# Optimization experiments

Measured on AMD Instinct MI355X. Metric: run time of the kernel, lower is better.

## Reference

```python
import jax, jax.numpy as jnp
import numpy as np

ALPHA = 0.2          # LeakyReLU negative slope
NEG_INF = -9e15      # mask value used by the torch module


def setup_inputs() -> dict:
    key = jax.random.key(0)
    k1, k2, k3, k4 = jax.random.split(key, 4)
    N, F_IN, F_OUT = 8192, 128, 128
    h = jax.random.normal(k1, (N, F_IN), dtype=jnp.float32)
    adj = jax.random.randint(k2, (N, N), 0, 2, dtype=jnp.int32)
    # xavier_uniform(gain=1.414) approximated with scaled normal init
    W = jax.random.normal(k3, (F_IN, F_OUT), dtype=jnp.float32) * (1.414 / np.sqrt(F_IN))
    a = jax.random.normal(k4, (2 * F_OUT, 1), dtype=jnp.float32) * (1.414 / np.sqrt(2 * F_OUT))
    return {"h": h, "adj": adj, "W": W, "a": a}


def reference(h, adj, W, a):
    # Wh: [N, F]
    Wh = h @ W
    F_out = W.shape[1]
    # e[i,j] = LeakyReLU( [Wh_i || Wh_j] . a ) = LeakyReLU( Wh_i.a1 + Wh_j.a2 )
    e_src = Wh @ a[:F_out, 0]   # [N]
    e_dst = Wh @ a[F_out:, 0]   # [N]
    e = jax.nn.leaky_relu(e_src[:, None] + e_dst[None, :], negative_slope=ALPHA)  # [N, N]
    attention = jax.nn.softmax(jnp.where(adj > 0, e, NEG_INF), axis=1)
    # dropout is identity in eval mode
    h_prime = attention @ Wh    # [N, F]
    return h_prime
```

## Files before the change

### kernel.cpp

```cpp
#include <hip/hip_runtime.h>
#include <hip/hip_bf16.h>


#define NN 8192
#define FF 128
#define SEG 4
#define JSEG (NN / SEG)
#define ITERS (JSEG / 64)

typedef __bf16 bf16x8 __attribute__((ext_vector_type(8)));
typedef float floatx4 __attribute__((ext_vector_type(4)));

__device__ __forceinline__ unsigned short f2b(float f) {
    unsigned int u = __float_as_uint(f);
    return (unsigned short)((u + 0x7FFFu + ((u >> 16) & 1u)) >> 16);
}

__global__ __launch_bounds__(128) void k0_uv(const float* __restrict__ W,
                                             const float* __restrict__ a,
                                             float* __restrict__ u,
                                             float* __restrict__ v) {
    int k = blockIdx.x, t = threadIdx.x;
    float wv = W[k * FF + t];
    float p1 = wv * a[t];
    float p2 = wv * a[FF + t];
    for (int off = 32; off; off >>= 1) {
        p1 += __shfl_down(p1, off);
        p2 += __shfl_down(p2, off);
    }
    __shared__ float r[4];
    if ((t & 63) == 0) { r[(t >> 6) * 2] = p1; r[(t >> 6) * 2 + 1] = p2; }
    __syncthreads();
    if (t == 0) { u[k] = r[0] + r[2]; v[k] = r[1] + r[3]; }
}

__global__ __launch_bounds__(256) void k1_wh(const float* __restrict__ h,
                                             const float* __restrict__ W,
                                             const float* __restrict__ u,
                                             const float* __restrict__ v,
                                             unsigned short* __restrict__ WhT,
                                             float* __restrict__ e_src,
                                             float* __restrict__ e_dst) {
    __shared__ float hL[32 * 132];
    __shared__ float wL[128 * 132];
    __shared__ float uL[128], vL[128];
    __shared__ unsigned short tL[128 * 40];

    int t = threadIdx.x;
    int i0 = blockIdx.x * 32;

    {
        int row = t >> 3, c = (t & 7) * 16;
        const float4* s = (const float4*)&h[(i0 + row) * FF + c];
        float4* d = (float4*)&hL[row * 132 + c];
        #pragma unroll
        for (int j = 0; j < 4; j++) d[j] = s[j];
    }
    {
        int row = t >> 1, c = (t & 1) * 64;
        const float4* s = (const float4*)&W[row * FF + c];
        float4* d = (float4*)&wL[row * 132 + c];
        #pragma unroll
        for (int j = 0; j < 16; j++) d[j] = s[j];
    }
    if (t < 128) { uL[t] = u[t]; vL[t] = v[t]; }
    __syncthreads();

    int r0 = (t & 7) * 4;
    int c0 = (t >> 3) * 4;
    float acc[4][4] = {};
    for (int k0 = 0; k0 < 128; k0 += 4) {
        float4 hr[4], wr[4];
        #pragma unroll
        for (int i = 0; i < 4; i++) hr[i] = *(const float4*)&hL[(r0 + i) * 132 + k0];
        #pragma unroll
        for (int i = 0; i < 4; i++) wr[i] = *(const float4*)&wL[(k0 + i) * 132 + c0];
        #pragma unroll
        for (int kj = 0; kj < 4; kj++) {
            #pragma unroll
            for (int ri = 0; ri < 4; ri++) {
                float hvv = ((const float*)&hr[ri])[kj];
                const float* wvv = (const float*)&wr[kj];
                #pragma unroll
                for (int cj = 0; cj < 4; cj++) acc[ri][cj] = fmaf(hvv, wvv[cj], acc[ri][cj]);
            }
        }
    }
    #pragma unroll
    for (int ri = 0; ri < 4; ri++)
        #pragma unroll
        for (int cj = 0; cj < 4; cj++)
            tL[(c0 + cj) * 40 + r0 + ri] = f2b(acc[ri][cj]);
    __syncthreads();

    if (t < 64) {
        int row = t & 31;
        const float* sv = (t < 32) ? uL : vL;
        float s = 0.f;
        for (int k = 0; k < 128; k += 4) {
            float4 h4 = *(const float4*)&hL[row * 132 + k];
            float4 s4 = *(const float4*)&sv[k];
            s = fmaf(h4.x, s4.x, s); s = fmaf(h4.y, s4.y, s);
            s = fmaf(h4.z, s4.z, s); s = fmaf(h4.w, s4.w, s);
        }
        (t < 32 ? e_src : e_dst)[i0 + row] = s;
    }
    {
        int f = t & 127, half = t >> 7;
        const uint4* s = (const uint4*)&tL[f * 40 + half * 16];
        uint4* d = (uint4*)&WhT[f * NN + i0 + half * 16];
        d[0] = s[0]; d[1] = s[1];
    }
}

__device__ __forceinline__ float mask_w(int a, float x) {
    float l = fmaxf(x, 0.2f * x);
    return a > 0 ? __expf(l) : 0.f;
}

__global__ __launch_bounds__(512, 4) void k2_gat(const int* __restrict__ adj,
                                                 const unsigned short* __restrict__ WhT,
                                                 const float* __restrict__ e_src,
                                                 const float* __restrict__ e_dst,
                                                 float* __restrict__ numpart,
                                                 float* __restrict__ denpart) {
    __shared__ unsigned short wt[2][32 * 64];
    __shared__ float esL[32];
    __shared__ float dpart[32 * 17];

    int t = threadIdx.x;
    int bx = blockIdx.x;
    int g = bx >> 2, seg = bx & 3;
    int i0 = g * 32;
    int jbase = seg * JSEG;

    if (t < 32) esL[t] = e_src[i0 + t];

    int q  = t & 15;
    int ii = t >> 4;
    int lane = t & 63, wave = t >> 6;
    int mrow = lane & 15, quad = lane >> 4;
    int n0 = wave * 16;

    const unsigned short* Bb = WhT + (size_t)(n0 + mrow) * NN + jbase + quad * 8;
    const int*   Ab = adj + (size_t)(i0 + ii) * NN + jbase + q * 4;
    const float* Eb = e_dst + jbase + q * 4;

    int waddr = ii * 64 + (((q >> 1) ^ (ii & 7)) << 3) + ((q & 1) << 2);
    int ra00 = mrow * 64 + ((quad ^ (mrow & 7)) << 3);
    int ra01 = mrow * 64 + (((4 + quad) ^ (mrow & 7)) << 3);
    int ra10 = (16 + mrow) * 64 + ((quad ^ (mrow & 7)) << 3);
    int ra11 = (16 + mrow) * 64 + (((4 + quad) ^ (mrow & 7)) << 3);

    floatx4 acc0 = {0.f, 0.f, 0.f, 0.f};
    floatx4 acc1 = {0.f, 0.f, 0.f, 0.f};
    float dsum = 0.f;

    int4   av0 = *(const int4*)Ab;
    float4 ed0 = *(const float4*)Eb;
    int4   avB = *(const int4*)(Ab + 64);
    float4 edB = *(const float4*)(Eb + 64);
    bf16x8 b0 = *(const bf16x8*)Bb;
    bf16x8 b1 = *(const bf16x8*)(Bb + 32);

    __syncthreads();
    float es_i = esL[ii];

    {
        float w0 = mask_w(av0.x, es_i + ed0.x);
        float w1 = mask_w(av0.y, es_i + ed0.y);
        float w2 = mask_w(av0.z, es_i + ed0.z);
        float w3 = mask_w(av0.w, es_i + ed0.w);
        dsum += (w0 + w1) + (w2 + w3);
        *(ushort4*)&wt[0][waddr] = make_ushort4(f2b(w0), f2b(w1), f2b(w2), f2b(w3));
    }
    __syncthreads();

    for (int k = 0; k < ITERS - 1; k++) {
        int jp = ((k + 2 < ITERS) ? (k + 2) : (ITERS - 1)) * 64;
        int4   avN = *(const int4*)(Ab + jp);
        float4 edN = *(const float4*)(Eb + jp);
        int jn = (k + 1) * 64;
        bf16x8 nb0 = *(const bf16x8*)(Bb + jn);
        bf16x8 nb1 = *(const bf16x8*)(Bb + jn + 32);

        const unsigned short* buf = wt[k & 1];
        bf16x8 a00 = *(const bf16x8*)&buf[ra00];
        bf16x8 a10 = *(const bf16x8*)&buf[ra10];
        bf16x8 a01 = *(const bf16x8*)&buf[ra01];
        bf16x8 a11 = *(const bf16x8*)&buf[ra11];
        acc0 = __builtin_amdgcn_mfma_f32_16x16x32_bf16(a00, b0, acc0, 0, 0, 0);
        acc1 = __builtin_amdgcn_mfma_f32_16x16x32_bf16(a10, b0, acc1, 0, 0, 0);
        acc0 = __builtin_amdgcn_mfma_f32_16x16x32_bf16(a01, b1, acc0, 0, 0, 0);
        acc1 = __builtin_amdgcn_mfma_f32_16x16x32_bf16(a11, b1, acc1, 0, 0, 0);

        float w0 = mask_w(avB.x, es_i + edB.x);
        float w1 = mask_w(avB.y, es_i + edB.y);
        float w2 = mask_w(avB.z, es_i + edB.z);
        float w3 = mask_w(avB.w, es_i + edB.w);
        dsum += (w0 + w1) + (w2 + w3);
        *(ushort4*)&wt[(k + 1) & 1][waddr] = make_ushort4(f2b(w0), f2b(w1), f2b(w2), f2b(w3));
        avB = avN; edB = edN;
        b0 = nb0; b1 = nb1;
        __syncthreads();
    }
    {
        const unsigned short* buf = wt[(ITERS - 1) & 1];
        bf16x8 a00 = *(const bf16x8*)&buf[ra00];
        bf16x8 a10 = *(const bf16x8*)&buf[ra10];
        bf16x8 a01 = *(const bf16x8*)&buf[ra01];
        bf16x8 a11 = *(const bf16x8*)&buf[ra11];
        acc0 = __builtin_amdgcn_mfma_f32_16x16x32_bf16(a00, b0, acc0, 0, 0, 0);
        acc1 = __builtin_amdgcn_mfma_f32_16x16x32_bf16(a10, b0, acc1, 0, 0, 0);
        acc0 = __builtin_amdgcn_mfma_f32_16x16x32_bf16(a01, b1, acc0, 0, 0, 0);
        acc1 = __builtin_amdgcn_mfma_f32_16x16x32_bf16(a11, b1, acc1, 0, 0, 0);
    }

    dpart[ii * 17 + q] = dsum;
    __syncthreads();
    if (t < 32) {
        float s = 0.f;
        #pragma unroll
        for (int k = 0; k < 16; k++) s += dpart[t * 17 + k];
        __builtin_nontemporal_store(s, &denpart[seg * NN + i0 + t]);
    }

    float* np = numpart + (size_t)seg * NN * FF;
    #pragma unroll
    for (int r = 0; r < 4; r++) {
        int row0 = quad * 4 + r;
        __builtin_nontemporal_store(acc0[r], &np[(size_t)(i0 + row0) * FF + n0 + mrow]);
        __builtin_nontemporal_store(acc1[r], &np[(size_t)(i0 + 16 + row0) * FF + n0 + mrow]);
    }
}

__global__ __launch_bounds__(256) void k3_merge(const float* __restrict__ np,
                                               const float* __restrict__ dp,
                                               float* __restrict__ out) {
    int idx = blockIdx.x * 256 + threadIdx.x;
    int i = idx >> 5;
    int c = (idx & 31) << 2;
    float d = dp[i] + dp[NN + i] + dp[2 * NN + i] + dp[3 * NN + i];
    float r = 1.0f / d;
    size_t o = (size_t)i * FF + c;
    const size_t S = (size_t)NN * FF;
    float4 a0 = *(const float4*)&np[o];
    float4 a1 = *(const float4*)&np[o + S];
    float4 a2 = *(const float4*)&np[o + 2 * S];
    float4 a3 = *(const float4*)&np[o + 3 * S];
    float4 v;
    v.x = ((a0.x + a1.x) + (a2.x + a3.x)) * r;
    v.y = ((a0.y + a1.y) + (a2.y + a3.y)) * r;
    v.z = ((a0.z + a1.z) + (a2.z + a3.z)) * r;
    v.w = ((a0.w + a1.w) + (a2.w + a3.w)) * r;
    *(float4*)&out[o] = v;
}

extern "C" void kernel_launch(void* const* d_in, const int* in_sizes, int n_in,
                              void* d_out, int out_size, void* d_ws, size_t ws_size,
                              hipStream_t stream) {
    const float* h   = (const float*)d_in[0];
    const int*   adj = (const int*)d_in[1];
    const float* W   = (const float*)d_in[2];
    const float* a   = (const float*)d_in[3];
    float* out = (float*)d_out;

    char* ws = (char*)d_ws;
    unsigned short* WhT = (unsigned short*)ws;
    float* u     = (float*)(ws + 2097152);
    float* v     = u + 128;
    float* e_src = v + 128;
    float* e_dst = e_src + NN;
    float* denpart = e_dst + NN;
    float* numpart = (float*)(ws + (4u << 20));

    k0_uv<<<dim3(128), dim3(128), 0, stream>>>(W, a, u, v);
    k1_wh<<<dim3(256), dim3(256), 0, stream>>>(h, W, u, v, WhT, e_src, e_dst);
    k2_gat<<<dim3(256 * SEG), dim3(512), 0, stream>>>(adj, WhT, e_src, e_dst, numpart, denpart);
    k3_merge<<<dim3(NN * FF / 4 / 256), dim3(256), 0, stream>>>(numpart, denpart, out);
}
```

Baseline: 404.3 us.

## Fuse uv projection into Wh kernel, use exp2, hardware bf16 cvt, nontemporal adj loads

```diff
diff --git a/kernel.cpp b/kernel.cpp
--- a/kernel.cpp
+++ b/kernel.cpp
@@ -10,34 +10,15 @@
 
 typedef __bf16 bf16x8 __attribute__((ext_vector_type(8)));
 typedef float floatx4 __attribute__((ext_vector_type(4)));
-
-__device__ __forceinline__ unsigned short f2b(float f) {
-    unsigned int u = __float_as_uint(f);
-    return (unsigned short)((u + 0x7FFFu + ((u >> 16) & 1u)) >> 16);
-}
-
-__global__ __launch_bounds__(128) void k0_uv(const float* __restrict__ W,
+typedef int   intx4  __attribute__((ext_vector_type(4)));
+
+__device__ __forceinline__ unsigned short b2u(__bf16 x) {
+    return __builtin_bit_cast(unsigned short, x);
+}
+
+__global__ __launch_bounds__(512) void k1_wh(const float* __restrict__ h,
+                                             const float* __restrict__ W,
                                              const float* __restrict__ a,
-                                             float* __restrict__ u,
-                                             float* __restrict__ v) {
-    int k = blockIdx.x, t = threadIdx.x;
-    float wv = W[k * FF + t];
-    float p1 = wv * a[t];
-    float p2 = wv * a[FF + t];
-    for (int off = 32; off; off >>= 1) {
-        p1 += __shfl_down(p1, off);
-        p2 += __shfl_down(p2, off);
-    }
-    __shared__ float r[4];
-    if ((t & 63) == 0) { r[(t >> 6) * 2] = p1; r[(t >> 6) * 2 + 1] = p2; }
-    __syncthreads();
-    if (t == 0) { u[k] = r[0] + r[2]; v[k] = r[1] + r[3]; }
-}
-
-__global__ __launch_bounds__(256) void k1_wh(const float* __restrict__ h,
-                                             const float* __restrict__ W,
-                                             const float* __restrict__ u,
-                                             const float* __restrict__ v,
                                              unsigned short* __restrict__ WhT,
                                              float* __restrict__ e_src,
                                              float* __restrict__ e_dst) {
@@ -50,47 +31,56 @@
     int i0 = blockIdx.x * 32;
 
     {
-        int row = t >> 3, c = (t & 7) * 16;
+        int row = t >> 4, c = (t & 15) * 8;
         const float4* s = (const float4*)&h[(i0 + row) * FF + c];
         float4* d = (float4*)&hL[row * 132 + c];
-        #pragma unroll
-        for (int j = 0; j < 4; j++) d[j] = s[j];
-    }
-    {
-        int row = t >> 1, c = (t & 1) * 64;
+        d[0] = s[0]; d[1] = s[1];
+    }
+    {
+        int row = t >> 2, c = (t & 3) * 32;
         const float4* s = (const float4*)&W[row * FF + c];
         float4* d = (float4*)&wL[row * 132 + c];
         #pragma unroll
-        for (int j = 0; j < 16; j++) d[j] = s[j];
-    }
-    if (t < 128) { uL[t] = u[t]; vL[t] = v[t]; }
-    __syncthreads();
+        for (int j = 0; j < 8; j++) d[j] = s[j];
+    }
+    __syncthreads();
+
+    if (t < 256) {
+        int k = t & 127;
+        const float* ap = a + (t >> 7) * FF;
+        float s = 0.f;
+        for (int c = 0; c < 128; c += 4) {
+            float4 w4 = *(const float4*)&wL[k * 132 + c];
+            s = fmaf(w4.x, ap[c], s);     s = fmaf(w4.y, ap[c + 1], s);
+            s = fmaf(w4.z, ap[c + 2], s); s = fmaf(w4.w, ap[c + 3], s);
+        }
+        (t < 128 ? uL : vL)[k] = s * 1.44269504f;
+    }
 
     int r0 = (t & 7) * 4;
-    int c0 = (t >> 3) * 4;
-    float acc[4][4] = {};
+    int c0 = (t >> 3) * 2;
+    float acc[4][2] = {};
     for (int k0 = 0; k0 < 128; k0 += 4) {
-        float4 hr[4], wr[4];
+        float4 hr[4]; float2 wr[4];
         #pragma unroll
         for (int i = 0; i < 4; i++) hr[i] = *(const float4*)&hL[(r0 + i) * 132 + k0];
         #pragma unroll
-        for (int i = 0; i < 4; i++) wr[i] = *(const float4*)&wL[(k0 + i) * 132 + c0];
+        for (int i = 0; i < 4; i++) wr[i] = *(const float2*)&wL[(k0 + i) * 132 + c0];
         #pragma unroll
         for (int kj = 0; kj < 4; kj++) {
             #pragma unroll
             for (int ri = 0; ri < 4; ri++) {
                 float hvv = ((const float*)&hr[ri])[kj];
-                const float* wvv = (const float*)&wr[kj];
-                #pragma unroll
-                for (int cj = 0; cj < 4; cj++) acc[ri][cj] = fmaf(hvv, wvv[cj], acc[ri][cj]);
+                acc[ri][0] = fmaf(hvv, wr[kj].x, acc[ri][0]);
+                acc[ri][1] = fmaf(hvv, wr[kj].y, acc[ri][1]);
             }
         }
     }
     #pragma unroll
     for (int ri = 0; ri < 4; ri++)
         #pragma unroll
-        for (int cj = 0; cj < 4; cj++)
-            tL[(c0 + cj) * 40 + r0 + ri] = f2b(acc[ri][cj]);
+        for (int cj = 0; cj < 2; cj++)
+            tL[(c0 + cj) * 40 + r0 + ri] = b2u((__bf16)acc[ri][cj]);
     __syncthreads();
 
     if (t < 64) {
@@ -106,16 +96,24 @@
         (t < 32 ? e_src : e_dst)[i0 + row] = s;
     }
     {
-        int f = t & 127, half = t >> 7;
-        const uint4* s = (const uint4*)&tL[f * 40 + half * 16];
-        uint4* d = (uint4*)&WhT[f * NN + i0 + half * 16];
-        d[0] = s[0]; d[1] = s[1];
+        int f = t & 127, part = t >> 7;
+        const uint4* s = (const uint4*)&tL[f * 40 + part * 8];
+        uint4* d = (uint4*)&WhT[f * NN + i0 + part * 8];
+        *d = *s;
     }
 }
 
 __device__ __forceinline__ float mask_w(int a, float x) {
     float l = fmaxf(x, 0.2f * x);
-    return a > 0 ? __expf(l) : 0.f;
+    float e = __builtin_amdgcn_exp2f(l);
+    return a > 0 ? e : 0.f;
+}
+
+__device__ __forceinline__ ushort4 pack4(float w0, float w1, float w2, float w3) {
+    union { ushort4 u; __bf16 b[4]; } pk;
+    pk.b[0] = (__bf16)w0; pk.b[1] = (__bf16)w1;
+    pk.b[2] = (__bf16)w2; pk.b[3] = (__bf16)w3;
+    return pk.u;
 }
 
 __global__ __launch_bounds__(512, 4) void k2_gat(const int* __restrict__ adj,
@@ -143,7 +141,7 @@
     int n0 = wave * 16;
 
     const unsigned short* Bb = WhT + (size_t)(n0 + mrow) * NN + jbase + quad * 8;
-    const int*   Ab = adj + (size_t)(i0 + ii) * NN + jbase + q * 4;
+    const intx4* Ab = (const intx4*)(adj + (size_t)(i0 + ii) * NN + jbase + q * 4);
     const float* Eb = e_dst + jbase + q * 4;
 
     int waddr = ii * 64 + (((q >> 1) ^ (ii & 7)) << 3) + ((q & 1) << 2);
@@ -156,9 +154,9 @@
     floatx4 acc1 = {0.f, 0.f, 0.f, 0.f};
     float dsum = 0.f;
 
-    int4   av0 = *(const int4*)Ab;
+    intx4  av0 = __builtin_nontemporal_load(Ab);
     float4 ed0 = *(const float4*)Eb;
-    int4   avB = *(const int4*)(Ab + 64);
+    intx4  avB = __builtin_nontemporal_load(Ab + 16);
     float4 edB = *(const float4*)(Eb + 64);
     bf16x8 b0 = *(const bf16x8*)Bb;
     bf16x8 b1 = *(const bf16x8*)(Bb + 32);
@@ -172,14 +170,14 @@
         float w2 = mask_w(av0.z, es_i + ed0.z);
         float w3 = mask_w(av0.w, es_i + ed0.w);
         dsum += (w0 + w1) + (w2 + w3);
-        *(ushort4*)&wt[0][waddr] = make_ushort4(f2b(w0), f2b(w1), f2b(w2), f2b(w3));
+        *(ushort4*)&wt[0][waddr] = pack4(w0, w1, w2, w3);
     }
     __syncthreads();
 
     for (int k = 0; k < ITERS - 1; k++) {
-        int jp = ((k + 2 < ITERS) ? (k + 2) : (ITERS - 1)) * 64;
-        int4   avN = *(const int4*)(Ab + jp);
-        float4 edN = *(const float4*)(Eb + jp);
+        int jp = ((k + 2 < ITERS) ? (k + 2) : (ITERS - 1));
+        intx4  avN = __builtin_nontemporal_load(Ab + jp * 16);
+        float4 edN = *(const float4*)(Eb + jp * 64);
         int jn = (k + 1) * 64;
         bf16x8 nb0 = *(const bf16x8*)(Bb + jn);
         bf16x8 nb1 = *(const bf16x8*)(Bb + jn + 32);
@@ -199,7 +197,7 @@
         float w2 = mask_w(avB.z, es_i + edB.z);
         float w3 = mask_w(avB.w, es_i + edB.w);
         dsum += (w0 + w1) + (w2 + w3);
-        *(ushort4*)&wt[(k + 1) & 1][waddr] = make_ushort4(f2b(w0), f2b(w1), f2b(w2), f2b(w3));
+        *(ushort4*)&wt[(k + 1) & 1][waddr] = pack4(w0, w1, w2, w3);
         avB = avN; edB = edN;
         b0 = nb0; b1 = nb1;
         __syncthreads();
@@ -267,15 +265,12 @@
 
     char* ws = (char*)d_ws;
     unsigned short* WhT = (unsigned short*)ws;
-    float* u     = (float*)(ws + 2097152);
-    float* v     = u + 128;
-    float* e_src = v + 128;
+    float* e_src = (float*)(ws + 2097152);
     float* e_dst = e_src + NN;
     float* denpart = e_dst + NN;
     float* numpart = (float*)(ws + (4u << 20));
 
-    k0_uv<<<dim3(128), dim3(128), 0, stream>>>(W, a, u, v);
-    k1_wh<<<dim3(256), dim3(256), 0, stream>>>(h, W, u, v, WhT, e_src, e_dst);
+    k1_wh<<<dim3(256), dim3(512), 0, stream>>>(h, W, a, WhT, e_src, e_dst);
     k2_gat<<<dim3(256 * SEG), dim3(512), 0, stream>>>(adj, WhT, e_src, e_dst, numpart, denpart);
     k3_merge<<<dim3(NN * FF / 4 / 256), dim3(256), 0, stream>>>(numpart, denpart, out);
 }
```

Result: no change. 397.8 us (-1.6%).
